# Performance work log

Measured on AMD Instinct MI355X. Metric: run time of the kernel, lower is better.

## Reference

```python
import jax, jax.numpy as jnp
import numpy as np

B, V, C = 2, 6, 96
D, H, W = 48, 48, 48
TH, TW = 96, 96
EPS = 1e-5


def _trilinear_sample_zeros(vol, gx, gy, gz):
    # vol: [B,C,D,H,W]; gx/gy/gz: normalized coords [D,H,W]; align_corners=False, zeros padding
    Dd, Hh, Ww = vol.shape[2], vol.shape[3], vol.shape[4]
    ix = ((gx + 1.0) * Ww - 1.0) * 0.5
    iy = ((gy + 1.0) * Hh - 1.0) * 0.5
    iz = ((gz + 1.0) * Dd - 1.0) * 0.5
    x0 = jnp.floor(ix); y0 = jnp.floor(iy); z0 = jnp.floor(iz)
    tx, ty, tz = ix - x0, iy - y0, iz - z0
    out = jnp.zeros(vol.shape, vol.dtype)
    for dz in (0, 1):
        for dy in (0, 1):
            for dx in (0, 1):
                xc, yc, zc = x0 + dx, y0 + dy, z0 + dz
                w = ((tx if dx else 1.0 - tx) * (ty if dy else 1.0 - ty)
                     * (tz if dz else 1.0 - tz))
                inb = ((xc >= 0) & (xc < Ww) & (yc >= 0) & (yc < Hh)
                       & (zc >= 0) & (zc < Dd))
                xi = jnp.clip(xc, 0, Ww - 1).astype(jnp.int32)
                yi = jnp.clip(yc, 0, Hh - 1).astype(jnp.int32)
                zi = jnp.clip(zc, 0, Dd - 1).astype(jnp.int32)
                val = vol[:, :, zi, yi, xi]  # [B,C,D,H,W]
                out = out + val * (w * inb)[None, None]
    return out


def _resize_bilinear(img, oh, ow):
    # torch F.interpolate(mode='bilinear', align_corners=False) semantics
    h, w = img.shape[-2], img.shape[-1]
    def idx(n_in, n_out):
        scale = n_in / n_out
        src = jnp.maximum(scale * (jnp.arange(n_out) + 0.5) - 0.5, 0.0)
        i0 = jnp.clip(jnp.floor(src).astype(jnp.int32), 0, n_in - 1)
        i1 = jnp.clip(i0 + 1, 0, n_in - 1)
        return i0, i1, (src - i0).astype(img.dtype)
    y0, y1, ty = idx(h, oh)
    x0, x1, tx = idx(w, ow)
    rows = img[..., y0, :] * (1.0 - ty)[:, None] + img[..., y1, :] * ty[:, None]
    return rows[..., x0] * (1.0 - tx) + rows[..., x1] * tx


def _project_one_view(vol, theta):
    # base grid per torch affine_grid(align_corners=False): pixel-center coords in [-1,1]
    zc = (jnp.arange(D) + 0.5) * (2.0 / D) - 1.0
    yc = (jnp.arange(H) + 0.5) * (2.0 / H) - 1.0
    xc = (jnp.arange(W) + 0.5) * (2.0 / W) - 1.0
    Z, Y, X = jnp.meshgrid(zc, yc, xc, indexing='ij')  # [D,H,W]
    c, s = jnp.cos(theta), jnp.sin(theta)
    gx = c * X + s * Z   # rotation about Y axis, rows [c,0,s],[0,1,0],[-s,0,c]
    gy = Y
    gz = -s * X + c * Z
    rotated = _trilinear_sample_zeros(vol, gx, gy, gz)  # [B,C,D,H,W]
    feat2d = rotated.mean(axis=2)                       # depth mean -> [B,C,H,W]
    return _resize_bilinear(feat2d, TH, TW)             # [B,C,TH,TW]


def _post(x, conv1_w, bn_gamma, bn_beta, conv2_w, conv2_b):
    dn = ('NCHW', 'OIHW', 'NCHW')
    x = jax.lax.conv_general_dilated(x, conv1_w, (1, 1), 'SAME', dimension_numbers=dn)
    mu = x.mean(axis=(0, 2, 3), keepdims=True)
    var = ((x - mu) ** 2).mean(axis=(0, 2, 3), keepdims=True)  # biased var, train-mode BN
    x = (x - mu) * jax.lax.rsqrt(var + EPS)
    x = x * bn_gamma[None, :, None, None] + bn_beta[None, :, None, None]
    x = jax.nn.gelu(x, approximate=False)
    x = jax.lax.conv_general_dilated(x, conv2_w, (1, 1), 'SAME', dimension_numbers=dn)
    return x + conv2_b[None, :, None, None]


def setup_inputs() -> dict:
    key = jax.random.key(0)
    k0, k1, k2 = jax.random.split(key, 3)
    voxel_tokens = jax.random.normal(k0, (B, D * H * W, C), jnp.float32)
    view_angles = jnp.linspace(0.0, 2.0 * np.pi, V + 1)[:-1].astype(jnp.float32)
    conv1_w = jax.random.normal(k1, (C, C, 3, 3), jnp.float32) / np.sqrt(C * 9.0)
    bn_gamma = jnp.ones((C,), jnp.float32)
    bn_beta = jnp.zeros((C,), jnp.float32)
    conv2_w = jax.random.normal(k2, (C, C, 1, 1), jnp.float32) / np.sqrt(C)
    conv2_b = jnp.zeros((C,), jnp.float32)
    return dict(voxel_tokens=voxel_tokens, view_angles=view_angles,
                conv1_w=conv1_w, bn_gamma=bn_gamma, bn_beta=bn_beta,
                conv2_w=conv2_w, conv2_b=conv2_b)


def reference(voxel_tokens, view_angles, conv1_w, bn_gamma, bn_beta, conv2_w, conv2_b):
    b = voxel_tokens.shape[0]
    vol = voxel_tokens.transpose(0, 2, 1).reshape(b, C, D, H, W)
    feats = jax.vmap(lambda th: _project_one_view(vol, th))(view_angles)  # [V,B,C,TH,TW]
    # BN stats are computed per-view (torch applies self.post inside the view loop)
    posted = jax.vmap(lambda f: _post(f, conv1_w, bn_gamma, bn_beta, conv2_w, conv2_b))(feats)
    return posted.transpose(1, 0, 2, 3, 4)  # [B,V,C,TH,TW]
```

## Files before the change

### kernel.cpp

```cpp
#include <hip/hip_runtime.h>
#include <math.h>

#define Bn 2
#define Vn 6
#define Cn 96
#define Dn 48
#define Hn 48
#define Wn 48
#define THn 96
#define TWn 96
#define EPSf 1e-5f

#define PD 98
#define NCI8 12

typedef __attribute__((ext_vector_type(8))) short s8v;
typedef __attribute__((ext_vector_type(4))) float f4v;
typedef __attribute__((ext_vector_type(2))) float f2v;

__device__ __forceinline__ unsigned short f2bf(float f) {
    unsigned int u = __builtin_bit_cast(unsigned int, f);
    u += 0x7FFFu + ((u >> 16) & 1u);
    return (unsigned short)(u >> 16);
}
__device__ __forceinline__ float bf2f(unsigned short h) {
    unsigned int u = ((unsigned int)h) << 16;
    return __builtin_bit_cast(float, u);
}
__device__ __forceinline__ void unpack8(uint4 r, float* f) {
    unsigned int w[4] = {r.x, r.y, r.z, r.w};
#pragma unroll
    for (int j = 0; j < 8; ++j)
        f[j] = bf2f((unsigned short)((w[j >> 1] >> ((j & 1) * 16)) & 0xFFFFu));
}
__device__ __forceinline__ void unpack8p(uint4 r, f2v* p) {
    unsigned int w[4] = {r.x, r.y, r.z, r.w};
#pragma unroll
    for (int i = 0; i < 4; ++i) {
        f2v t;
        t.x = __builtin_bit_cast(float, w[i] << 16);
        t.y = __builtin_bit_cast(float, w[i] & 0xFFFF0000u);
        p[i] = t;
    }
}
__device__ __forceinline__ uint4 pack8(const unsigned short* o) {
    uint4 pk;
    pk.x = (unsigned int)o[0] | ((unsigned int)o[1] << 16);
    pk.y = (unsigned int)o[2] | ((unsigned int)o[3] << 16);
    pk.z = (unsigned int)o[4] | ((unsigned int)o[5] << 16);
    pk.w = (unsigned int)o[6] | ((unsigned int)o[7] << 16);
    return pk;
}

__device__ __forceinline__ float gelu_f(float y) {
    float z = y * 0.70710678118654752f;
    float a = fabsf(z);
    float t = __builtin_amdgcn_rcpf(fmaf(0.3275911f, a, 1.0f));
    float e = __builtin_amdgcn_exp2f(-1.4426950408889634f * a * a);
    float p = t * fmaf(t, fmaf(t, fmaf(t, fmaf(t, 1.061405429f,
                                               -1.453152027f),
                                       1.421413741f),
                               -0.284496736f),
                       0.254829592f);
    float er = fmaf(-p, e, 1.0f);
    er = copysignf(er, z);
    return 0.5f * y * (1.0f + er);
}

__global__ __launch_bounds__(256) void k_pre(const float* __restrict__ tokens,
                                             unsigned short* __restrict__ tokB,
                                             const float* __restrict__ w1,
                                             const float* __restrict__ w2,
                                             unsigned short* __restrict__ wAtP,
                                             unsigned short* __restrict__ wCP,
                                             const float* __restrict__ angles,
                                             float4* __restrict__ wtabW,
                                             int4* __restrict__ wtabO) {
    if (blockIdx.x < 10368) {
        int idx = blockIdx.x * 256 + threadIdx.x;
        size_t base = (size_t)idx * 8;
        float4 f0 = *(const float4*)(tokens + base);
        float4 f1 = *(const float4*)(tokens + base + 4);
        unsigned short o[8] = {f2bf(f0.x), f2bf(f0.y), f2bf(f0.z), f2bf(f0.w),
                               f2bf(f1.x), f2bf(f1.y), f2bf(f1.z), f2bf(f1.w)};
        *(uint4*)(&tokB[base]) = pack8(o);
    } else if (blockIdx.x < 10728) {
        int i = (blockIdx.x - 10368) * 256 + threadIdx.x;
        if (i < 82944) {
            int e = i & 7;
            int u = i >> 3;
            int co = u % 96;
            int u2 = u / 96;
            int ci8 = u2 % NCI8;
            int tap = u2 / NCI8;
            wAtP[i] = f2bf(w1[(co * 96 + ci8 * 8 + e) * 9 + tap]);
        } else if (i < 92160) {
            int j = i - 82944;
            int e = j & 7;
            int u = j >> 3;
            int co = u % 96;
            int ci8 = u / 96;
            wCP[j] = f2bf(w2[co * 96 + ci8 * 8 + e]);
        }
    } else {
        int e = (blockIdx.x - 10728) * 256 + threadIdx.x;
        if (e >= 13824) return;
        int z = e % 48;
        int r = e / 48;
        int x = r % 48;
        int v = r / 48;

        float th = angles[v];
        float ct = cosf(th), st = sinf(th);
        float xr = (float)x + 0.5f - 24.0f;
        float zr = (float)z + 0.5f - 24.0f;
        float ix = ct * xr + st * zr + 23.5f;
        float iz = -st * xr + ct * zr + 23.5f;

        float x0f = floorf(ix), z0f = floorf(iz);
        float tx = ix - x0f, tz = iz - z0f;
        int x0 = (int)x0f, z0 = (int)z0f;
        float wx[2] = {1.0f - tx, tx};
        float wz[2] = {1.0f - tz, tz};

        float w[4];
        int o[4];
#pragma unroll
        for (int dz = 0; dz < 2; ++dz) {
            int zc = z0 + dz;
            bool zin = (zc >= 0) && (zc < Dn);
            int zi = min(max(zc, 0), Dn - 1);
#pragma unroll
            for (int dx = 0; dx < 2; ++dx) {
                int xc = x0 + dx;
                bool xin = (xc >= 0) && (xc < Wn);
                int xi = min(max(xc, 0), Wn - 1);
                int k = dz * 2 + dx;
                w[k] = wx[dx] * wz[dz] * ((zin && xin) ? 1.0f : 0.0f) * (1.0f / 48.0f);
                o[k] = (zi * 221184 + xi * 96) * 2;
            }
        }
        wtabW[e] = (float4){w[0], w[1], w[2], w[3]};
        wtabO[e] = (int4){o[0], o[1], o[2], o[3]};
    }
}

__global__ __launch_bounds__(256) void k_feat7(const unsigned short* __restrict__ tokB,
                                               const float4* __restrict__ wtabW,
                                               const int4* __restrict__ wtabO,
                                               unsigned short* __restrict__ featP) {
    int gid = blockIdx.x;
    int xcd = gid & 7;
    int pos = gid >> 3;
    int vblk = xcd * 648 + pos;
    int group = vblk / 9;
    int inner = vblk - group * 9;
    int v = group % 6;
    int by = group / 6;
    int y = by % 48;
    int b = by / 48;
    int vb = v * 2 + b;

    int t = threadIdx.x;
    int l = t & 63;
    int h = l >> 4;
    int s0 = inner * 64 + (t >> 6) * 16 + (l & 15);
    int c8 = s0 % NCI8;
    int x = s0 / NCI8;

    int tb0 = (v * 48 + x) * 48 + h * 12;
    const float4* tw = wtabW + tb0;
    const int4* to = wtabO + tb0;
    const char* tb = (const char*)tokB +
                     ((size_t)b * 10616832 + (size_t)y * 4608 + c8 * 8) * 2;

    f2v af[4];
#pragma unroll
    for (int i = 0; i < 4; ++i) af[i] = (f2v){0.f, 0.f};

#pragma unroll 4
    for (int k = 0; k < 12; ++k) {
        float4 w = tw[k];
        int4 o = to[k];
        uint4 r0 = *(const uint4*)(tb + o.x);
        uint4 r1 = *(const uint4*)(tb + o.y);
        uint4 r2 = *(const uint4*)(tb + o.z);
        uint4 r3 = *(const uint4*)(tb + o.w);
        f2v p0[4], p1[4], p2[4], p3[4];
        unpack8p(r0, p0); unpack8p(r1, p1); unpack8p(r2, p2); unpack8p(r3, p3);
        f2v wx = (f2v){w.x, w.x}, wy = (f2v){w.y, w.y};
        f2v wz = (f2v){w.z, w.z}, ww = (f2v){w.w, w.w};
#pragma unroll
        for (int i = 0; i < 4; ++i) {
            af[i] = __builtin_elementwise_fma(wx, p0[i], af[i]);
            af[i] = __builtin_elementwise_fma(wy, p1[i], af[i]);
            af[i] = __builtin_elementwise_fma(wz, p2[i], af[i]);
            af[i] = __builtin_elementwise_fma(ww, p3[i], af[i]);
        }
    }
#pragma unroll
    for (int i = 0; i < 4; ++i) {
        af[i].x += __shfl_xor(af[i].x, 16);
        af[i].y += __shfl_xor(af[i].y, 16);
        af[i].x += __shfl_xor(af[i].x, 32);
        af[i].y += __shfl_xor(af[i].y, 32);
    }

    if (h == 0) {
        unsigned short o[8];
#pragma unroll
        for (int j = 0; j < 8; ++j) o[j] = f2bf((j & 1) ? af[j >> 1].y : af[j >> 1].x);
        size_t off = (((size_t)vb * Hn + y) * NCI8 + c8) * Wn + x;
        *(uint4*)(&featP[off * 8]) = pack8(o);
    }
}

__global__ __launch_bounds__(256) void k_resize(const unsigned short* __restrict__ featP,
                                                unsigned short* __restrict__ rz) {
    if (blockIdx.x >= 5184) {
        int hid = (blockIdx.x - 5184) * 256 + threadIdx.x;
        if (hid >= 55872) return;
        int p = hid % 388;
        int r2 = hid / 388;
        int c8 = r2 % NCI8;
        int vb = r2 / NCI8;
        int py, px;
        if (p < 98)      { py = 0;  px = p; }
        else if (p < 196){ py = 97; px = p - 98; }
        else { int q = p - 196; py = 1 + (q >> 1); px = (q & 1) ? 97 : 0; }
        size_t off = (((size_t)vb * PD + py) * NCI8 + c8) * PD + px;
        *(uint4*)(&rz[off * 8]) = (uint4){0u, 0u, 0u, 0u};
        return;
    }
    int idx = blockIdx.x * 256 + threadIdx.x;
    int x = idx % TWn;
    int r = idx / TWn;
    int c8i = r % NCI8; r /= NCI8;
    int y = r % THn;
    int vb = r / THn;

    float sy = fmaxf(0.5f * (y + 0.5f) - 0.5f, 0.0f);
    int y0 = min((int)sy, Hn - 1);
    int y1 = min(y0 + 1, Hn - 1);
    float ty = sy - (float)y0;
    float sx = fmaxf(0.5f * (x + 0.5f) - 0.5f, 0.0f);
    int x0 = min((int)sx, Wn - 1);
    int x1 = min(x0 + 1, Wn - 1);
    float tx = sx - (float)x0;

    const unsigned short* fb = featP + ((size_t)vb * Hn * NCI8 + c8i) * Wn * 8;
    const unsigned short* r0 = fb + (size_t)y0 * (NCI8 * Wn * 8);
    const unsigned short* r1 = fb + (size_t)y1 * (NCI8 * Wn * 8);
    uint4 q00 = *(const uint4*)(r0 + (size_t)x0 * 8);
    uint4 q01 = *(const uint4*)(r0 + (size_t)x1 * 8);
    uint4 q10 = *(const uint4*)(r1 + (size_t)x0 * 8);
    uint4 q11 = *(const uint4*)(r1 + (size_t)x1 * 8);
    float f00[8], f01[8], f10[8], f11[8];
    unpack8(q00, f00); unpack8(q01, f01); unpack8(q10, f10); unpack8(q11, f11);

    float w00 = (1.f - ty) * (1.f - tx), w01 = (1.f - ty) * tx;
    float w10 = ty * (1.f - tx),         w11 = ty * tx;

    unsigned short o[8];
#pragma unroll
    for (int j = 0; j < 8; ++j)
        o[j] = f2bf(w00 * f00[j] + w01 * f01[j] + w10 * f10[j] + w11 * f11[j]);

    size_t off = (((size_t)vb * PD + (y + 1)) * NCI8 + c8i) * PD + (x + 1);
    *(uint4*)(&rz[off * 8]) = pack8(o);
}

__global__ __launch_bounds__(256) void k_conv1(const unsigned short* __restrict__ rz,
                                               const unsigned short* __restrict__ wAtP,
                                               unsigned short* __restrict__ co1) {
    int blk = blockIdx.x;
    int n0 = blk * 64;
    int vb = n0 / 9216;
    int nl0 = n0 - vb * 9216;

    int t = threadIdx.x;
    int wv = t >> 6;
    int ch = wv & 1;
    int ns = wv >> 1;
    int l = t & 63;
    int l15 = l & 15, q = l >> 4;

    int nt0 = nl0 + ns * 32;
    int nl[2];
    const unsigned short* pB[2];
#pragma unroll
    for (int i = 0; i < 2; ++i) {
        nl[i] = nt0 + i * 16 + l15;
        int y = nl[i] / 96, x = nl[i] - y * 96;
        pB[i] = rz + ((((size_t)vb * PD + y) * NCI8) * PD + x) * 8;
    }

    f4v acc[2][3];
#pragma unroll
    for (int i = 0; i < 2; ++i)
#pragma unroll
        for (int mt = 0; mt < 3; ++mt) acc[i][mt] = (f4v){0.f, 0.f, 0.f, 0.f};

#pragma unroll
    for (int ks = 0; ks < 3; ++ks) {
        int ci8 = ks * 4 + q;
        const unsigned short* pb0 = pB[0] + (size_t)ci8 * (PD * 8);
        const unsigned short* pb1 = pB[1] + (size_t)ci8 * (PD * 8);
        const unsigned short* pa = wAtP + ((size_t)ci8 * 96 + ch * 48 + l15) * 8;
#pragma unroll
        for (int tap = 0; tap < 9; ++tap) {
            int dy = tap / 3, dx = tap % 3;
            size_t toff = ((size_t)dy * (NCI8 * PD) + dx) * 8;
            s8v b0 = *(const s8v*)(pb0 + toff);
            s8v b1 = *(const s8v*)(pb1 + toff);
            const unsigned short* ap = pa + (size_t)tap * (NCI8 * 96 * 8);
#pragma unroll
            for (int mt = 0; mt < 3; ++mt) {
                s8v a = *(const s8v*)(ap + (size_t)mt * (16 * 8));
                acc[0][mt] = __builtin_amdgcn_mfma_f32_16x16x32_bf16(a, b0, acc[0][mt], 0, 0, 0);
                acc[1][mt] = __builtin_amdgcn_mfma_f32_16x16x32_bf16(a, b1, acc[1][mt], 0, 0, 0);
            }
        }
    }

#pragma unroll
    for (int i = 0; i < 2; ++i) {
#pragma unroll
        for (int mt = 0; mt < 3; ++mt) {
            int co0 = ch * 48 + mt * 16 + q * 4;
            ushort4 pk;
            pk.x = f2bf(acc[i][mt][0]); pk.y = f2bf(acc[i][mt][1]);
            pk.z = f2bf(acc[i][mt][2]); pk.w = f2bf(acc[i][mt][3]);
            size_t off = (((size_t)vb * NCI8 + (co0 >> 3)) * 9216 + nl[i]) * 8 + (co0 & 7);
            *(ushort4*)(&co1[off]) = pk;
        }
    }
}

__global__ __launch_bounds__(256) void k_stats1(const unsigned short* __restrict__ co1,
                                                float* __restrict__ part) {
    int g = blockIdx.x >> 4;
    int chunk = blockIdx.x & 15;
    int v = g / NCI8;
    int c8 = g % NCI8;
    int t = threadIdx.x;

    float s[8] = {0,0,0,0,0,0,0,0}, ss[8] = {0,0,0,0,0,0,0,0};
    int m0 = chunk * 1152;
    for (int m = m0 + t; m < m0 + 1152; m += 256) {
        int bb = m / 9216;
        int n = m - bb * 9216;
        const unsigned short* p = co1 + (((size_t)(v * 2 + bb) * NCI8 + c8) * 9216 + n) * 8;
        uint4 raw = *(const uint4*)p;
        float f[8];
        unpack8(raw, f);
#pragma unroll
        for (int j = 0; j < 8; ++j) { s[j] += f[j]; ss[j] += f[j] * f[j]; }
    }
#pragma unroll
    for (int off = 1; off < 64; off <<= 1) {
#pragma unroll
        for (int j = 0; j < 8; ++j) {
            s[j]  += __shfl_xor(s[j],  off);
            ss[j] += __shfl_xor(ss[j], off);
        }
    }
    __shared__ float rs[4][8], rss[4][8];
    int wv = t >> 6;
    if ((t & 63) == 0) {
#pragma unroll
        for (int j = 0; j < 8; ++j) { rs[wv][j] = s[j]; rss[wv][j] = ss[j]; }
    }
    __syncthreads();
    if (t < 8) {
        int j = t;
        part[(size_t)blockIdx.x * 16 + j]     = rs[0][j] + rs[1][j] + rs[2][j] + rs[3][j];
        part[(size_t)blockIdx.x * 16 + 8 + j] = rss[0][j] + rss[1][j] + rss[2][j] + rss[3][j];
    }
}

__global__ __launch_bounds__(256) void k_conv2(const unsigned short* __restrict__ co1,
                                               const unsigned short* __restrict__ wCP,
                                               const float* __restrict__ part,
                                               const float* __restrict__ gamma,
                                               const float* __restrict__ beta,
                                               const float* __restrict__ b2,
                                               float* __restrict__ out) {
    __shared__ float ssc[96], ssh[96], sbias[96];
    __shared__ float sOut[96 * 65];

    int blk = blockIdx.x;
    int n0 = blk * 64;
    int vb = n0 / 9216;
    int nl0 = n0 - vb * 9216;
    int v = vb >> 1, b = vb & 1;

    int t = threadIdx.x;
    int wv = t >> 6;
    int l = t & 63;
    int l15 = l & 15, q = l >> 4;

    if (t < 96) {
        int c8 = t >> 3, j = t & 7;
        int g = v * NCI8 + c8;
        float S = 0.f, SS = 0.f;
#pragma unroll
        for (int c = 0; c < 16; ++c) {
            const float* pp = part + ((size_t)g * 16 + c) * 16;
            S += pp[j];
            SS += pp[8 + j];
        }
        const float invN = 1.0f / (float)(Bn * THn * TWn);
        float mu = S * invN;
        float var = SS * invN - mu * mu;
        float rstd = rsqrtf(fmaxf(var, 0.0f) + EPSf);
        float sc = rstd * gamma[t];
        ssc[t] = sc;
        ssh[t] = beta[t] - mu * sc;
        sbias[t] = b2[t];
    }
    __syncthreads();

    int n = nl0 + wv * 16 + l15;

    f4v acc[6];
#pragma unroll
    for (int mt = 0; mt < 6; ++mt) acc[mt] = (f4v){0.f, 0.f, 0.f, 0.f};

#pragma unroll
    for (int ks = 0; ks < 3; ++ks) {
        int ci8 = ks * 4 + q;
        int ci0 = ci8 * 8;
        float sc[8], sh[8];
#pragma unroll
        for (int j = 0; j < 8; ++j) { sc[j] = ssc[ci0 + j]; sh[j] = ssh[ci0 + j]; }

        const unsigned short* pb = co1 + (((size_t)vb * NCI8 + ci8) * 9216 + n) * 8;
        uint4 raw = *(const uint4*)pb;
        float f[8];
        unpack8(raw, f);
        unsigned short o[8];
#pragma unroll
        for (int j = 0; j < 8; ++j) {
            float yv = f[j] * sc[j] + sh[j];
            o[j] = f2bf(gelu_f(yv));
        }
        s8v bfr = __builtin_bit_cast(s8v, pack8(o));

        const unsigned short* pa = wCP + ((size_t)ci8 * 96 + l15) * 8;
#pragma unroll
        for (int mt = 0; mt < 6; ++mt) {
            s8v a = *(const s8v*)(pa + (size_t)mt * (16 * 8));
            acc[mt] = __builtin_amdgcn_mfma_f32_16x16x32_bf16(a, bfr, acc[mt], 0, 0, 0);
        }
    }

    int nloc = wv * 16 + l15;
#pragma unroll
    for (int mt = 0; mt < 6; ++mt) {
        int co0 = mt * 16 + q * 4;
#pragma unroll
        for (int reg = 0; reg < 4; ++reg) {
            int co = co0 + reg;
            sOut[co * 65 + nloc] = acc[mt][reg] + sbias[co];
        }
    }
    __syncthreads();

    size_t obase = ((size_t)(b * Vn + v) * Cn) * 9216 + nl0;
#pragma unroll
    for (int r = 0; r < 6; ++r) {
        int cid = r * 256 + t;
        int row = cid >> 4;
        int chunk = cid & 15;
        float4 vv = *(const float4*)(&sOut[row * 65 + chunk * 4]);
        *(float4*)(&out[obase + (size_t)row * 9216 + chunk * 4]) = vv;
    }
}

extern "C" void kernel_launch(void* const* d_in, const int* in_sizes, int n_in,
                              void* d_out, int out_size, void* d_ws, size_t ws_size,
                              hipStream_t stream) {
    const float* tokens = (const float*)d_in[0];
    const float* angles = (const float*)d_in[1];
    const float* w1     = (const float*)d_in[2];
    const float* gamma  = (const float*)d_in[3];
    const float* beta   = (const float*)d_in[4];
    const float* w2     = (const float*)d_in[5];
    const float* b2     = (const float*)d_in[6];
    float* out = (float*)d_out;

    char* ws = (char*)d_ws;
    unsigned short* featP = (unsigned short*)(ws);
    float* part           = (float*)(ws);
    unsigned short* tokB  = (unsigned short*)(ws + 5308416);
    unsigned short* rz    = (unsigned short*)(ws + 5308416);
    unsigned short* co1   = (unsigned short*)(ws + 27436032);
    float4* wtabW         = (float4*)(ws + 47775744);
    int4*  wtabO          = (int4*)(ws + 47996928);
    unsigned short* wAtP  = (unsigned short*)(ws + 48669696);
    unsigned short* wCP   = (unsigned short*)(ws + 48835584);

    k_pre<<<10782, 256, 0, stream>>>(tokens, tokB, w1, w2, wAtP, wCP,
                                     angles, wtabW, wtabO);
    k_feat7<<<5184, 256, 0, stream>>>(tokB, wtabW, wtabO, featP);
    k_resize<<<5403, 256, 0, stream>>>(featP, rz);
    k_conv1<<<1728, 256, 0, stream>>>(rz, wAtP, co1);
    k_stats1<<<1152, 256, 0, stream>>>(co1, part);
    k_conv2<<<1728, 256, 0, stream>>>(co1, wCP, part, gamma, beta, b2, out);
}
```

Measured before the change: 261.0 us.

## Stage y-slice in LDS and compute all views per block for projection

```diff
diff --git a/kernel.cpp b/kernel.cpp
--- a/kernel.cpp
+++ b/kernel.cpp
@@ -72,10 +72,7 @@
                                              const float* __restrict__ w1,
                                              const float* __restrict__ w2,
                                              unsigned short* __restrict__ wAtP,
-                                             unsigned short* __restrict__ wCP,
-                                             const float* __restrict__ angles,
-                                             float4* __restrict__ wtabW,
-                                             int4* __restrict__ wtabO) {
+                                             unsigned short* __restrict__ wCP) {
     if (blockIdx.x < 10368) {
         int idx = blockIdx.x * 256 + threadIdx.x;
         size_t base = (size_t)idx * 8;
@@ -84,7 +81,7 @@
         unsigned short o[8] = {f2bf(f0.x), f2bf(f0.y), f2bf(f0.z), f2bf(f0.w),
                                f2bf(f1.x), f2bf(f1.y), f2bf(f1.z), f2bf(f1.w)};
         *(uint4*)(&tokB[base]) = pack8(o);
-    } else if (blockIdx.x < 10728) {
+    } else {
         int i = (blockIdx.x - 10368) * 256 + threadIdx.x;
         if (i < 82944) {
             int e = i & 7;
@@ -102,117 +99,89 @@
             int ci8 = u / 96;
             wCP[j] = f2bf(w2[co * 96 + ci8 * 8 + e]);
         }
-    } else {
-        int e = (blockIdx.x - 10728) * 256 + threadIdx.x;
-        if (e >= 13824) return;
-        int z = e % 48;
-        int r = e / 48;
-        int x = r % 48;
-        int v = r / 48;
-
-        float th = angles[v];
-        float ct = cosf(th), st = sinf(th);
-        float xr = (float)x + 0.5f - 24.0f;
-        float zr = (float)z + 0.5f - 24.0f;
-        float ix = ct * xr + st * zr + 23.5f;
-        float iz = -st * xr + ct * zr + 23.5f;
-
+    }
+}
+
+__global__ __launch_bounds__(288) void k_feat8(const unsigned short* __restrict__ tokB,
+                                               const float* __restrict__ angles,
+                                               unsigned short* __restrict__ featP) {
+    __shared__ uint4 sl[48 * 50];
+
+    int gid = blockIdx.x;
+    int xcd = gid & 7;
+    int pos = gid >> 3;
+    int vblk = xcd * 144 + pos;
+    int c8 = vblk % NCI8;
+    int by = vblk / NCI8;
+    int y = by % 48;
+    int b = by / 48;
+
+    int t = threadIdx.x;
+
+    const unsigned short* src0 = tokB + (size_t)b * 10616832 + (size_t)y * 4608 + c8 * 8;
+#pragma unroll
+    for (int s = 0; s < 8; ++s) {
+        int p = s * 288 + t;
+        int z = p / 48, x = p - z * 48;
+        sl[z * 50 + x] = *(const uint4*)(src0 + (size_t)z * 221184 + (size_t)x * 96);
+    }
+    __syncthreads();
+
+    int v = t / 48;
+    int x = t - v * 48;
+
+    float th = angles[v];
+    float ct = cosf(th), st = sinf(th);
+    float xr = (float)x - 23.5f;
+    float ix = ct * xr - 23.5f * st + 23.5f;
+    float iz = -st * xr - 23.5f * ct + 23.5f;
+
+    f2v af[4];
+#pragma unroll
+    for (int i = 0; i < 4; ++i) af[i] = (f2v){0.f, 0.f};
+
+#pragma unroll 2
+    for (int z = 0; z < 48; ++z) {
         float x0f = floorf(ix), z0f = floorf(iz);
         float tx = ix - x0f, tz = iz - z0f;
         int x0 = (int)x0f, z0 = (int)z0f;
-        float wx[2] = {1.0f - tx, tx};
-        float wz[2] = {1.0f - tz, tz};
-
-        float w[4];
-        int o[4];
-#pragma unroll
-        for (int dz = 0; dz < 2; ++dz) {
-            int zc = z0 + dz;
-            bool zin = (zc >= 0) && (zc < Dn);
-            int zi = min(max(zc, 0), Dn - 1);
-#pragma unroll
-            for (int dx = 0; dx < 2; ++dx) {
-                int xc = x0 + dx;
-                bool xin = (xc >= 0) && (xc < Wn);
-                int xi = min(max(xc, 0), Wn - 1);
-                int k = dz * 2 + dx;
-                w[k] = wx[dx] * wz[dz] * ((zin && xin) ? 1.0f : 0.0f) * (1.0f / 48.0f);
-                o[k] = (zi * 221184 + xi * 96) * 2;
-            }
-        }
-        wtabW[e] = (float4){w[0], w[1], w[2], w[3]};
-        wtabO[e] = (int4){o[0], o[1], o[2], o[3]};
-    }
-}
-
-__global__ __launch_bounds__(256) void k_feat7(const unsigned short* __restrict__ tokB,
-                                               const float4* __restrict__ wtabW,
-                                               const int4* __restrict__ wtabO,
-                                               unsigned short* __restrict__ featP) {
-    int gid = blockIdx.x;
-    int xcd = gid & 7;
-    int pos = gid >> 3;
-    int vblk = xcd * 648 + pos;
-    int group = vblk / 9;
-    int inner = vblk - group * 9;
-    int v = group % 6;
-    int by = group / 6;
-    int y = by % 48;
-    int b = by / 48;
+        float wx0 = (1.f - tx) * (((x0 >= 0) && (x0 < 48)) ? 1.f : 0.f);
+        float wx1 = tx * (((x0 >= -1) && (x0 < 47)) ? 1.f : 0.f);
+        float wz0 = (1.f - tz) * (((z0 >= 0) && (z0 < 48)) ? 1.f : 0.f);
+        float wz1 = tz * (((z0 >= -1) && (z0 < 47)) ? 1.f : 0.f);
+        int xi0 = min(max(x0, 0), 47), xi1 = min(max(x0 + 1, 0), 47);
+        int zi0 = min(max(z0, 0), 47), zi1 = min(max(z0 + 1, 0), 47);
+
+        uint4 r00 = sl[zi0 * 50 + xi0];
+        uint4 r01 = sl[zi0 * 50 + xi1];
+        uint4 r10 = sl[zi1 * 50 + xi0];
+        uint4 r11 = sl[zi1 * 50 + xi1];
+        f2v p00[4], p01[4], p10[4], p11[4];
+        unpack8p(r00, p00); unpack8p(r01, p01);
+        unpack8p(r10, p10); unpack8p(r11, p11);
+        float w00 = wz0 * wx0, w01 = wz0 * wx1;
+        float w10 = wz1 * wx0, w11 = wz1 * wx1;
+        f2v v00 = (f2v){w00, w00}, v01 = (f2v){w01, w01};
+        f2v v10 = (f2v){w10, w10}, v11 = (f2v){w11, w11};
+#pragma unroll
+        for (int i = 0; i < 4; ++i) {
+            af[i] = __builtin_elementwise_fma(v00, p00[i], af[i]);
+            af[i] = __builtin_elementwise_fma(v01, p01[i], af[i]);
+            af[i] = __builtin_elementwise_fma(v10, p10[i], af[i]);
+            af[i] = __builtin_elementwise_fma(v11, p11[i], af[i]);
+        }
+        ix += st;
+        iz += ct;
+    }
+
+    const float s = 1.0f / 48.0f;
+    unsigned short o[8];
+#pragma unroll
+    for (int j = 0; j < 8; ++j)
+        o[j] = f2bf(((j & 1) ? af[j >> 1].y : af[j >> 1].x) * s);
     int vb = v * 2 + b;
-
-    int t = threadIdx.x;
-    int l = t & 63;
-    int h = l >> 4;
-    int s0 = inner * 64 + (t >> 6) * 16 + (l & 15);
-    int c8 = s0 % NCI8;
-    int x = s0 / NCI8;
-
-    int tb0 = (v * 48 + x) * 48 + h * 12;
-    const float4* tw = wtabW + tb0;
-    const int4* to = wtabO + tb0;
-    const char* tb = (const char*)tokB +
-                     ((size_t)b * 10616832 + (size_t)y * 4608 + c8 * 8) * 2;
-
-    f2v af[4];
-#pragma unroll
-    for (int i = 0; i < 4; ++i) af[i] = (f2v){0.f, 0.f};
-
-#pragma unroll 4
-    for (int k = 0; k < 12; ++k) {
-        float4 w = tw[k];
-        int4 o = to[k];
-        uint4 r0 = *(const uint4*)(tb + o.x);
-        uint4 r1 = *(const uint4*)(tb + o.y);
-        uint4 r2 = *(const uint4*)(tb + o.z);
-        uint4 r3 = *(const uint4*)(tb + o.w);
-        f2v p0[4], p1[4], p2[4], p3[4];
-        unpack8p(r0, p0); unpack8p(r1, p1); unpack8p(r2, p2); unpack8p(r3, p3);
-        f2v wx = (f2v){w.x, w.x}, wy = (f2v){w.y, w.y};
-        f2v wz = (f2v){w.z, w.z}, ww = (f2v){w.w, w.w};
-#pragma unroll
-        for (int i = 0; i < 4; ++i) {
-            af[i] = __builtin_elementwise_fma(wx, p0[i], af[i]);
-            af[i] = __builtin_elementwise_fma(wy, p1[i], af[i]);
-            af[i] = __builtin_elementwise_fma(wz, p2[i], af[i]);
-            af[i] = __builtin_elementwise_fma(ww, p3[i], af[i]);
-        }
-    }
-#pragma unroll
-    for (int i = 0; i < 4; ++i) {
-        af[i].x += __shfl_xor(af[i].x, 16);
-        af[i].y += __shfl_xor(af[i].y, 16);
-        af[i].x += __shfl_xor(af[i].x, 32);
-        af[i].y += __shfl_xor(af[i].y, 32);
-    }
-
-    if (h == 0) {
-        unsigned short o[8];
-#pragma unroll
-        for (int j = 0; j < 8; ++j) o[j] = f2bf((j & 1) ? af[j >> 1].y : af[j >> 1].x);
-        size_t off = (((size_t)vb * Hn + y) * NCI8 + c8) * Wn + x;
-        *(uint4*)(&featP[off * 8]) = pack8(o);
-    }
+    size_t off = (((size_t)vb * Hn + y) * NCI8 + c8) * Wn + x;
+    *(uint4*)(&featP[off * 8]) = pack8(o);
 }
 
 __global__ __launch_bounds__(256) void k_resize(const unsigned short* __restrict__ featP,
@@ -496,14 +465,11 @@
     unsigned short* tokB  = (unsigned short*)(ws + 5308416);
     unsigned short* rz    = (unsigned short*)(ws + 5308416);
     unsigned short* co1   = (unsigned short*)(ws + 27436032);
-    float4* wtabW         = (float4*)(ws + 47775744);
-    int4*  wtabO          = (int4*)(ws + 47996928);
     unsigned short* wAtP  = (unsigned short*)(ws + 48669696);
     unsigned short* wCP   = (unsigned short*)(ws + 48835584);
 
-    k_pre<<<10782, 256, 0, stream>>>(tokens, tokB, w1, w2, wAtP, wCP,
-                                     angles, wtabW, wtabO);
-    k_feat7<<<5184, 256, 0, stream>>>(tokB, wtabW, wtabO, featP);
+    k_pre<<<10728, 256, 0, stream>>>(tokens, tokB, w1, w2, wAtP, wCP);
+    k_feat8<<<1152, 288, 0, stream>>>(tokB, angles, featP);
     k_resize<<<5403, 256, 0, stream>>>(featP, rz);
     k_conv1<<<1728, 256, 0, stream>>>(rz, wAtP, co1);
     k_stats1<<<1152, 256, 0, stream>>>(co1, part);
```

Result: slower. 273.5 us (+4.8%).

## Fuse BN statistics into conv1 epilogue and add tiny per-view reduce kernel

Applied to the files above, without the earlier changes.

```diff
diff --git a/kernel.cpp b/kernel.cpp
--- a/kernel.cpp
+++ b/kernel.cpp
@@ -272,7 +272,11 @@
 
 __global__ __launch_bounds__(256) void k_conv1(const unsigned short* __restrict__ rz,
                                                const unsigned short* __restrict__ wAtP,
-                                               unsigned short* __restrict__ co1) {
+                                               unsigned short* __restrict__ co1,
+                                               float* __restrict__ part2) {
+    __shared__ float sS[4][48];
+    __shared__ float sQ[4][48];
+
     int blk = blockIdx.x;
     int n0 = blk * 64;
     int vb = n0 / 9216;
@@ -335,55 +339,67 @@
             *(ushort4*)(&co1[off]) = pk;
         }
     }
-}
-
-__global__ __launch_bounds__(256) void k_stats1(const unsigned short* __restrict__ co1,
-                                                float* __restrict__ part) {
-    int g = blockIdx.x >> 4;
-    int chunk = blockIdx.x & 15;
-    int v = g / NCI8;
-    int c8 = g % NCI8;
+
+#pragma unroll
+    for (int mt = 0; mt < 3; ++mt) {
+#pragma unroll
+        for (int reg = 0; reg < 4; ++reg) {
+            float a0 = acc[0][mt][reg], a1 = acc[1][mt][reg];
+            float xs = a0 + a1;
+            float xq = a0 * a0 + a1 * a1;
+#pragma unroll
+            for (int off = 1; off < 16; off <<= 1) {
+                xs += __shfl_xor(xs, off);
+                xq += __shfl_xor(xq, off);
+            }
+            if (l15 == 0) {
+                sS[wv][mt * 16 + q * 4 + reg] = xs;
+                sQ[wv][mt * 16 + q * 4 + reg] = xq;
+            }
+        }
+    }
+    __syncthreads();
+    if (t < 96) {
+        int c2 = t / 48, cl = t % 48;
+        part2[(size_t)blk * 192 + t]      = sS[c2][cl] + sS[c2 + 2][cl];
+        part2[(size_t)blk * 192 + 96 + t] = sQ[c2][cl] + sQ[c2 + 2][cl];
+    }
+}
+
+__global__ __launch_bounds__(256) void k_statsR(const float* __restrict__ part2,
+                                                const float* __restrict__ gamma,
+                                                const float* __restrict__ beta,
+                                                float* __restrict__ scale,
+                                                float* __restrict__ shift) {
+    __shared__ float red[192];
+    int v = blockIdx.x;
     int t = threadIdx.x;
-
-    float s[8] = {0,0,0,0,0,0,0,0}, ss[8] = {0,0,0,0,0,0,0,0};
-    int m0 = chunk * 1152;
-    for (int m = m0 + t; m < m0 + 1152; m += 256) {
-        int bb = m / 9216;
-        int n = m - bb * 9216;
-        const unsigned short* p = co1 + (((size_t)(v * 2 + bb) * NCI8 + c8) * 9216 + n) * 8;
-        uint4 raw = *(const uint4*)p;
-        float f[8];
-        unpack8(raw, f);
-#pragma unroll
-        for (int j = 0; j < 8; ++j) { s[j] += f[j]; ss[j] += f[j] * f[j]; }
-    }
-#pragma unroll
-    for (int off = 1; off < 64; off <<= 1) {
-#pragma unroll
-        for (int j = 0; j < 8; ++j) {
-            s[j]  += __shfl_xor(s[j],  off);
-            ss[j] += __shfl_xor(ss[j], off);
-        }
-    }
-    __shared__ float rs[4][8], rss[4][8];
-    int wv = t >> 6;
-    if ((t & 63) == 0) {
-#pragma unroll
-        for (int j = 0; j < 8; ++j) { rs[wv][j] = s[j]; rss[wv][j] = ss[j]; }
+    if (t < 192) {
+        float a = 0.f;
+#pragma unroll 2
+        for (int bb = 0; bb < 2; ++bb) {
+            const float* p = part2 + ((size_t)(v * 2 + bb) * 144) * 192 + t;
+            for (int c = 0; c < 144; ++c) a += p[(size_t)c * 192];
+        }
+        red[t] = a;
     }
     __syncthreads();
-    if (t < 8) {
-        int j = t;
-        part[(size_t)blockIdx.x * 16 + j]     = rs[0][j] + rs[1][j] + rs[2][j] + rs[3][j];
-        part[(size_t)blockIdx.x * 16 + 8 + j] = rss[0][j] + rss[1][j] + rss[2][j] + rss[3][j];
+    if (t < 96) {
+        float S = red[t], Q = red[96 + t];
+        const float invN = 1.0f / (float)(Bn * THn * TWn);
+        float mu = S * invN;
+        float var = Q * invN - mu * mu;
+        float rstd = rsqrtf(fmaxf(var, 0.0f) + EPSf);
+        float sc = rstd * gamma[t];
+        scale[v * 96 + t] = sc;
+        shift[v * 96 + t] = beta[t] - mu * sc;
     }
 }
 
 __global__ __launch_bounds__(256) void k_conv2(const unsigned short* __restrict__ co1,
                                                const unsigned short* __restrict__ wCP,
-                                               const float* __restrict__ part,
-                                               const float* __restrict__ gamma,
-                                               const float* __restrict__ beta,
+                                               const float* __restrict__ scale,
+                                               const float* __restrict__ shift,
                                                const float* __restrict__ b2,
                                                float* __restrict__ out) {
     __shared__ float ssc[96], ssh[96], sbias[96];
@@ -401,22 +417,8 @@
     int l15 = l & 15, q = l >> 4;
 
     if (t < 96) {
-        int c8 = t >> 3, j = t & 7;
-        int g = v * NCI8 + c8;
-        float S = 0.f, SS = 0.f;
-#pragma unroll
-        for (int c = 0; c < 16; ++c) {
-            const float* pp = part + ((size_t)g * 16 + c) * 16;
-            S += pp[j];
-            SS += pp[8 + j];
-        }
-        const float invN = 1.0f / (float)(Bn * THn * TWn);
-        float mu = S * invN;
-        float var = SS * invN - mu * mu;
-        float rstd = rsqrtf(fmaxf(var, 0.0f) + EPSf);
-        float sc = rstd * gamma[t];
-        ssc[t] = sc;
-        ssh[t] = beta[t] - mu * sc;
+        ssc[t] = scale[v * 96 + t];
+        ssh[t] = shift[v * 96 + t];
         sbias[t] = b2[t];
     }
     __syncthreads();
@@ -492,7 +494,7 @@
 
     char* ws = (char*)d_ws;
     unsigned short* featP = (unsigned short*)(ws);
-    float* part           = (float*)(ws);
+    float* part2          = (float*)(ws);
     unsigned short* tokB  = (unsigned short*)(ws + 5308416);
     unsigned short* rz    = (unsigned short*)(ws + 5308416);
     unsigned short* co1   = (unsigned short*)(ws + 27436032);
@@ -500,12 +502,14 @@
     int4*  wtabO          = (int4*)(ws + 47996928);
     unsigned short* wAtP  = (unsigned short*)(ws + 48669696);
     unsigned short* wCP   = (unsigned short*)(ws + 48835584);
+    float* scale = (float*)(ws + 48854016);
+    float* shift = (float*)(ws + 48856320);
 
     k_pre<<<10782, 256, 0, stream>>>(tokens, tokB, w1, w2, wAtP, wCP,
                                      angles, wtabW, wtabO);
     k_feat7<<<5184, 256, 0, stream>>>(tokB, wtabW, wtabO, featP);
     k_resize<<<5403, 256, 0, stream>>>(featP, rz);
-    k_conv1<<<1728, 256, 0, stream>>>(rz, wAtP, co1);
-    k_stats1<<<1152, 256, 0, stream>>>(co1, part);
-    k_conv2<<<1728, 256, 0, stream>>>(co1, wCP, part, gamma, beta, b2, out);
-}
+    k_conv1<<<1728, 256, 0, stream>>>(rz, wAtP, co1, part2);
+    k_statsR<<<6, 256, 0, stream>>>(part2, gamma, beta, scale, shift);
+    k_conv2<<<1728, 256, 0, stream>>>(co1, wCP, scale, shift, b2, out);
+}
```

Result: no change. 263.5 us (+1.0%).
